# Kernel optimization log

Measured on AMD Instinct MI355X. Metric: run time of the kernel, lower is better.

Reference implementation:

```python
import jax, jax.numpy as jnp
import numpy as np

V, C, H, T, B, D = 32000, 768, 12, 1024, 2, 4
HID = C // 2
FF = 4 * C
HD = C // H


def _ln(x, s, b):
    m = jnp.mean(x, axis=-1, keepdims=True)
    v = jnp.mean((x - m) ** 2, axis=-1, keepdims=True)
    return (x - m) * jax.lax.rsqrt(v + 1e-5) * s + b


def setup_inputs() -> dict:
    key = jax.random.key(0)
    ks = jax.random.split(key, 12)
    nrm = lambda k, shp: 0.02 * jax.random.normal(k, shp, dtype=jnp.float32)
    return {
        "idx": jax.random.randint(ks[0], (B, T), 0, V),
        "tok_emb": nrm(ks[1], (V, C)),
        "pos_emb": nrm(ks[2], (T, C)),
        "r_w1": nrm(ks[3], (C, HID)), "r_b1": jnp.zeros((HID,), jnp.float32),
        "r_w2": nrm(ks[4], (HID, D)), "r_b2": jnp.zeros((D,), jnp.float32),
        "ln1_s": jnp.ones((C,), jnp.float32), "ln1_b": jnp.zeros((C,), jnp.float32),
        "qkv_w": nrm(ks[5], (C, 3 * C)),
        "proj_w": nrm(ks[6], (C, C)), "proj_b": jnp.zeros((C,), jnp.float32),
        "ln2_s": jnp.ones((C,), jnp.float32), "ln2_b": jnp.zeros((C,), jnp.float32),
        "f_w1": nrm(ks[7], (C, FF)), "f_b1": jnp.zeros((FF,), jnp.float32),
        "f_w2": nrm(ks[8], (FF, C)), "f_b2": jnp.zeros((C,), jnp.float32),
        "lnf_s": jnp.ones((C,), jnp.float32), "lnf_b": jnp.zeros((C,), jnp.float32),
        "head_w": nrm(ks[9], (V, C)),  # torch Linear weight [out, in]
    }


def reference(idx, tok_emb, pos_emb, r_w1, r_b1, r_w2, r_b2,
              ln1_s, ln1_b, qkv_w, proj_w, proj_b, ln2_s, ln2_b,
              f_w1, f_b1, f_w2, f_b2, lnf_s, lnf_b, head_w):
    # embeddings
    x = tok_emb[idx] + pos_emb[None, :, :]  # [B,T,C]

    # depth router (eval mode: hard one-hot argmax, k=1)
    rh = jax.nn.relu(x @ r_w1 + r_b1)
    r_logits = rh @ r_w2 + r_b2  # [B,T,D]
    w = jax.nn.one_hot(jnp.argmax(r_logits, axis=-1), D, dtype=x.dtype)  # [B,T,D]

    causal = jnp.tril(jnp.ones((T, T), dtype=bool))
    scale = 1.0 / np.sqrt(HD).astype(np.float32)

    def block(z):
        # pre-norm attention
        y = _ln(z, ln1_s, ln1_b)
        qkv = y @ qkv_w  # [B,T,3C]
        q, k, v = jnp.split(qkv, 3, axis=-1)
        q = q.reshape(B, T, H, HD)
        k = k.reshape(B, T, H, HD)
        v = v.reshape(B, T, H, HD)
        att = jnp.einsum('bqhd,bkhd->bhqk', q, k) * scale
        att = jnp.where(causal, att, -jnp.inf)
        att = jax.nn.softmax(att, axis=-1)
        o = jnp.einsum('bhqk,bkhd->bqhd', att, v).reshape(B, T, C)
        z = z + (o @ proj_w + proj_b)
        # pre-norm FFN (dropout inactive in eval)
        y2 = _ln(z, ln2_s, ln2_b)
        ff = jax.nn.gelu(y2 @ f_w1 + f_b1, approximate=False) @ f_w2 + f_b2
        return z + ff

    # depth-d output = block applied (d+1) times; accumulate with router weight
    out = jnp.zeros_like(x)
    h = x
    for d in range(D):
        h = block(h)
        out = out + w[:, :, d:d + 1] * h

    xf = _ln(out, lnf_s, lnf_b)
    logits = xf @ head_w.T  # [B,T,V]
    return logits
```

## Files before the change

kernel.cpp:

```cpp
#include <hip/hip_runtime.h>
#include <hip/hip_bf16.h>

typedef unsigned short u16;
typedef __bf16 bf16x8 __attribute__((ext_vector_type(8)));
typedef float f32x4 __attribute__((ext_vector_type(4)));

#define DEVINL __device__ __forceinline__

DEVINL u16 f2b(float f){
  unsigned u = __float_as_uint(f);
  u += 0x7FFFu + ((u >> 16) & 1u);
  return (u16)(u >> 16);
}
DEVINL float b2f(u16 b){ return __uint_as_float(((unsigned)b) << 16); }

DEVINL void gload16(const void* g, void* l){
  __builtin_amdgcn_global_load_lds(
      (const __attribute__((address_space(1))) unsigned*)g,
      (__attribute__((address_space(3))) unsigned*)l, 16, 0, 0);
}

__global__ __launch_bounds__(256) void k_embed(const int* __restrict__ idx,
    const float* __restrict__ tok, const float* __restrict__ pos, float* __restrict__ h){
  int r = blockIdx.x, t = threadIdx.x;
  int token = idx[r];
  const float* tr = tok + (long)token * 768;
  const float* pr = pos + (long)(r & 1023) * 768;
  float* hr = h + (long)r * 768;
  hr[t]       = tr[t]       + pr[t];
  hr[t + 256] = tr[t + 256] + pr[t + 256];
  hr[t + 512] = tr[t + 512] + pr[t + 512];
}

__global__ __launch_bounds__(256) void k_ln(const float* __restrict__ X,
    const float* __restrict__ s, const float* __restrict__ b, u16* __restrict__ Y){
  int r = blockIdx.x, t = threadIdx.x;
  const float* x = X + (long)r * 768;
  float v0 = x[t], v1 = x[t + 256], v2 = x[t + 512];
  float sum = v0 + v1 + v2;
  __shared__ float tmp[4];
  #pragma unroll
  for (int o = 32; o; o >>= 1) sum += __shfl_xor(sum, o);
  int wave = t >> 6;
  if ((t & 63) == 0) tmp[wave] = sum;
  __syncthreads();
  sum = tmp[0] + tmp[1] + tmp[2] + tmp[3];
  float m = sum * (1.f / 768.f);
  float d0 = v0 - m, d1 = v1 - m, d2 = v2 - m;
  float sq = d0 * d0 + d1 * d1 + d2 * d2;
  #pragma unroll
  for (int o = 32; o; o >>= 1) sq += __shfl_xor(sq, o);
  __syncthreads();
  if ((t & 63) == 0) tmp[wave] = sq;
  __syncthreads();
  sq = tmp[0] + tmp[1] + tmp[2] + tmp[3];
  float rs = rsqrtf(sq * (1.f / 768.f) + 1e-5f);
  u16* y = Y + (long)r * 768;
  y[t]       = f2b(d0 * rs * s[t]       + b[t]);
  y[t + 256] = f2b(d1 * rs * s[t + 256] + b[t + 256]);
  y[t + 512] = f2b(d2 * rs * s[t + 512] + b[t + 512]);
}

__global__ __launch_bounds__(256) void k_wt(const float* __restrict__ W, u16* __restrict__ Wt,
                                            int K, int N){
  __shared__ float tile[32][33];
  int kb = blockIdx.x * 32, nb = blockIdx.y * 32;
  int tx = threadIdx.x & 31, ty = threadIdx.x >> 5;
  #pragma unroll
  for (int i = 0; i < 32; i += 8) tile[ty + i][tx] = W[(long)(kb + ty + i) * N + nb + tx];
  __syncthreads();
  #pragma unroll
  for (int i = 0; i < 32; i += 8) Wt[(long)(nb + ty + i) * K + kb + tx] = f2b(tile[tx][ty + i]);
}

__global__ __launch_bounds__(256) void k_conv(const float* __restrict__ W, u16* __restrict__ O, long n4){
  long i = (long)blockIdx.x * 256 + threadIdx.x;
  if (i >= n4) return;
  float4 v = ((const float4*)W)[i];
  unsigned lo = (unsigned)f2b(v.x) | ((unsigned)f2b(v.y) << 16);
  unsigned hi = (unsigned)f2b(v.z) | ((unsigned)f2b(v.w) << 16);
  ((uint2*)O)[i] = make_uint2(lo, hi);
}

__global__ __launch_bounds__(256) void k_r1(const float* __restrict__ A, const float* __restrict__ B,
    const float* __restrict__ bias, float* __restrict__ C){
  __shared__ float As[64][17];
  __shared__ float Bs[16][65];
  int r0 = blockIdx.x * 64, c0 = blockIdx.y * 64;
  int t = threadIdx.x;
  int tx = t & 15, ty = t >> 4;
  float acc[4][4] = {};
  for (int k0 = 0; k0 < 768; k0 += 16){
    #pragma unroll
    for (int i = 0; i < 4; i++){ int e = i * 256 + t; As[e >> 4][e & 15] = A[(long)(r0 + (e >> 4)) * 768 + k0 + (e & 15)]; }
    #pragma unroll
    for (int i = 0; i < 4; i++){ int e = i * 256 + t; Bs[e >> 6][e & 63] = B[(long)(k0 + (e >> 6)) * 384 + c0 + (e & 63)]; }
    __syncthreads();
    #pragma unroll
    for (int kk = 0; kk < 16; kk++){
      float a[4], bb[4];
      #pragma unroll
      for (int i = 0; i < 4; i++) a[i] = As[ty * 4 + i][kk];
      #pragma unroll
      for (int j = 0; j < 4; j++) bb[j] = Bs[kk][tx * 4 + j];
      #pragma unroll
      for (int i = 0; i < 4; i++)
        #pragma unroll
        for (int j = 0; j < 4; j++) acc[i][j] += a[i] * bb[j];
    }
    __syncthreads();
  }
  #pragma unroll
  for (int i = 0; i < 4; i++)
    #pragma unroll
    for (int j = 0; j < 4; j++){
      int rr = r0 + ty * 4 + i, cc = c0 + tx * 4 + j;
      float v = acc[i][j] + bias[cc];
      C[(long)rr * 384 + cc] = v > 0.f ? v : 0.f;
    }
}

__global__ __launch_bounds__(64) void k_r2(const float* __restrict__ rh, const float* __restrict__ w2,
    const float* __restrict__ b2, int* __restrict__ sel){
  int tkn = blockIdx.x, l = threadIdx.x;
  float s0 = 0, s1 = 0, s2 = 0, s3 = 0;
  const float* r = rh + (long)tkn * 384;
  for (int k = l; k < 384; k += 64){
    float rv = r[k];
    float4 w = ((const float4*)w2)[k];
    s0 += rv * w.x; s1 += rv * w.y; s2 += rv * w.z; s3 += rv * w.w;
  }
  #pragma unroll
  for (int o = 32; o; o >>= 1){
    s0 += __shfl_xor(s0, o); s1 += __shfl_xor(s1, o);
    s2 += __shfl_xor(s2, o); s3 += __shfl_xor(s3, o);
  }
  if (l == 0){
    float v[4] = { s0 + b2[0], s1 + b2[1], s2 + b2[2], s3 + b2[3] };
    int am = 0; float bv = v[0];
    #pragma unroll
    for (int j = 1; j < 4; j++) if (v[j] > bv){ bv = v[j]; am = j; }
    sel[tkn] = am;
  }
}

__global__ __launch_bounds__(256) void k_attn(
    const u16* __restrict__ qkv, const u16* __restrict__ Vt, u16* __restrict__ o){
  __shared__ __align__(16) u16 Klds[64][64];
  __shared__ __align__(16) u16 Vlds[64][64];
  __shared__ __align__(16) u16 Plds[4][16][72];
  int qt = blockIdx.x, bh = blockIdx.y;
  int b = bh / 12, hh = bh % 12;
  int t = threadIdx.x, w = t >> 6, lane = t & 63;
  int lr = lane & 15, koct = lane >> 4;
  int q0 = qt * 64 + w * 16;
  const u16* Qrow = qkv + ((long)(b * 1024 + q0 + lr)) * 2304 + hh * 64;
  bf16x8 qf[2];
  qf[0] = __builtin_bit_cast(bf16x8, *(const uint4*)&Qrow[koct * 8]);
  qf[1] = __builtin_bit_cast(bf16x8, *(const uint4*)&Qrow[32 + koct * 8]);
  f32x4 oacc[4] = {};
  float m_run[4], l_run[4];
  #pragma unroll
  for (int r = 0; r < 4; r++){ m_run[r] = -1e30f; l_run[r] = 0.f; }
  int srow8 = lane >> 3, scolb = (lane & 7) * 16;
  const char* Kbase = (const char*)(qkv + (long)b * 1024 * 2304 + 768 + hh * 64);
  const char* Vbase = (const char*)(Vt + (long)bh * 64 * 1024);
  for (int kvt = 0; kvt <= qt; ++kvt){
    #pragma unroll
    for (int i = 0; i < 2; i++){
      int row = w * 16 + i * 8 + srow8;
      int sb = scolb ^ ((row & 7) << 4);
      gload16(Kbase + (long)(kvt * 64 + row) * 4608 + sb, &Klds[w * 16 + i * 8][0]);
    }
    #pragma unroll
    for (int i = 0; i < 2; i++){
      int row = w * 16 + i * 8 + srow8;
      int sb = scolb ^ ((row & 7) << 4);
      gload16(Vbase + (long)row * 2048 + kvt * 128 + sb, &Vlds[w * 16 + i * 8][0]);
    }
    __syncthreads();
    f32x4 sacc[4] = {};
    #pragma unroll
    for (int j = 0; j < 4; j++){
      #pragma unroll
      for (int f = 0; f < 2; f++){
        int row = 16 * j + lr;
        bf16x8 kf = __builtin_bit_cast(bf16x8, *(const uint4*)(
            (const char*)&Klds[0][0] + row * 128 + ((64 * f + koct * 16) ^ ((row & 7) << 4))));
        sacc[j] = __builtin_amdgcn_mfma_f32_16x16x32_bf16(qf[f], kf, sacc[j], 0, 0, 0);
      }
    }
    bool diag = (kvt == qt);
    float p[4][4];
    #pragma unroll
    for (int r = 0; r < 4; r++){
      int qg = q0 + 4 * koct + r;
      float vj[4];
      #pragma unroll
      for (int j = 0; j < 4; j++){
        int kvg = kvt * 64 + 16 * j + lr;
        float v = sacc[j][r] * 0.125f;
        vj[j] = (!diag || kvg <= qg) ? v : -1e30f;
      }
      float mx = fmaxf(fmaxf(vj[0], vj[1]), fmaxf(vj[2], vj[3]));
      #pragma unroll
      for (int s = 1; s < 16; s <<= 1) mx = fmaxf(mx, __shfl_xor(mx, s));
      float mn = fmaxf(m_run[r], mx);
      float sc = __expf(m_run[r] - mn);
      float rs = 0.f;
      #pragma unroll
      for (int j = 0; j < 4; j++){ p[j][r] = __expf(vj[j] - mn); rs += p[j][r]; }
      #pragma unroll
      for (int s = 1; s < 16; s <<= 1) rs += __shfl_xor(rs, s);
      l_run[r] = l_run[r] * sc + rs;
      m_run[r] = mn;
      #pragma unroll
      for (int j = 0; j < 4; j++) oacc[j][r] *= sc;
    }
    #pragma unroll
    for (int r = 0; r < 4; r++)
      #pragma unroll
      for (int j = 0; j < 4; j++)
        Plds[w][4 * koct + r][16 * j + lr] = f2b(p[j][r]);
    bf16x8 pf[2];
    pf[0] = __builtin_bit_cast(bf16x8, *(const uint4*)&Plds[w][lr][koct * 8]);
    pf[1] = __builtin_bit_cast(bf16x8, *(const uint4*)&Plds[w][lr][32 + koct * 8]);
    #pragma unroll
    for (int j = 0; j < 4; j++){
      #pragma unroll
      for (int f = 0; f < 2; f++){
        int row = 16 * j + lr;
        bf16x8 vf = __builtin_bit_cast(bf16x8, *(const uint4*)(
            (const char*)&Vlds[0][0] + row * 128 + ((64 * f + koct * 16) ^ ((row & 7) << 4))));
        oacc[j] = __builtin_amdgcn_mfma_f32_16x16x32_bf16(pf[f], vf, oacc[j], 0, 0, 0);
      }
    }
    __syncthreads();
  }
  float inv[4];
  #pragma unroll
  for (int r = 0; r < 4; r++) inv[r] = 1.f / l_run[r];
  #pragma unroll
  for (int j = 0; j < 4; j++){
    #pragma unroll
    for (int r = 0; r < 4; r++){
      int tq = b * 1024 + q0 + 4 * koct + r;
      o[(long)tq * 768 + hh * 64 + 16 * j + lr] = f2b(oacc[j][r] * inv[r]);
    }
  }
}

__global__ __launch_bounds__(256) void k_redln(const float* __restrict__ P, int nparts,
    const float* __restrict__ bias, const float* __restrict__ resid, float* __restrict__ outh,
    const float* __restrict__ ls, const float* __restrict__ lb, u16* __restrict__ Y,
    const int* __restrict__ sel, float* __restrict__ outb, int d){
  int r = blockIdx.x, t = threadIdx.x;
  float v0, v1, v2;
  {
    float a0 = bias[t]       + resid[(long)r * 768 + t];
    float a1 = bias[t + 256] + resid[(long)r * 768 + t + 256];
    float a2 = bias[t + 512] + resid[(long)r * 768 + t + 512];
    for (int p = 0; p < nparts; p++){
      const float* pr = P + ((long)p * 2048 + r) * 768;
      a0 += pr[t]; a1 += pr[t + 256]; a2 += pr[t + 512];
    }
    v0 = a0; v1 = a1; v2 = a2;
  }
  float* hr = outh + (long)r * 768;
  hr[t] = v0; hr[t + 256] = v1; hr[t + 512] = v2;
  if (sel && sel[r] == d){
    float* orow = outb + (long)r * 768;
    orow[t] = v0; orow[t + 256] = v1; orow[t + 512] = v2;
  }
  float sum = v0 + v1 + v2;
  __shared__ float tmp[4];
  #pragma unroll
  for (int o = 32; o; o >>= 1) sum += __shfl_xor(sum, o);
  int wave = t >> 6;
  if ((t & 63) == 0) tmp[wave] = sum;
  __syncthreads();
  sum = tmp[0] + tmp[1] + tmp[2] + tmp[3];
  float m = sum * (1.f / 768.f);
  float d0 = v0 - m, d1 = v1 - m, d2 = v2 - m;
  float sq = d0 * d0 + d1 * d1 + d2 * d2;
  #pragma unroll
  for (int o = 32; o; o >>= 1) sq += __shfl_xor(sq, o);
  __syncthreads();
  if ((t & 63) == 0) tmp[wave] = sq;
  __syncthreads();
  sq = tmp[0] + tmp[1] + tmp[2] + tmp[3];
  float rs = rsqrtf(sq * (1.f / 768.f) + 1e-5f);
  u16* y = Y + (long)r * 768;
  y[t]       = f2b(d0 * rs * ls[t]       + lb[t]);
  y[t + 256] = f2b(d1 * rs * ls[t + 256] + lb[t + 256]);
  y[t + 512] = f2b(d2 * rs * ls[t + 512] + lb[t + 512]);
}

__global__ __launch_bounds__(64) void k_gemm1(
    const u16* __restrict__ A, int lda, long s1A, long s2A,
    const u16* __restrict__ B, int ldb, long s1B, long s2B,
    void* Cv, int ldc, long s1C, long s2C,
    const float* __restrict__ bias,
    const float* __restrict__ resid, int ldr,
    int K, int zdiv, int ksegK, int flags, u16* __restrict__ vtbuf){
  __shared__ __align__(16) u16 As[2][64][32];
  __shared__ __align__(16) u16 Bs[2][64][32];
  int lane = threadIdx.x;
  int bx = blockIdx.x, by = blockIdx.y, bz = blockIdx.z;
  if (flags & 16){
    int nx = gridDim.x, nwg = nx * gridDim.y;
    int lin = by * nx + bx;
    int q = nwg >> 3;
    int nl = (lin & 7) * q + (lin >> 3);
    bx = nl % nx; by = nl / nx;
  }
  int row0 = bx * 64, col0 = by * 64;
  int zq = bz / zdiv, zr = bz % zdiv;
  A += zq * s2A + (long)zr * s1A;
  B += zq * s2B + (long)zr * s1B;
  long coff = zq * s2C + (long)zr * s1C;
  int kstart = 0, Klim = K;
  if (ksegK > 0){ kstart = bz * ksegK; Klim = kstart + ksegK; }
  f32x4 acc[4][4] = {};
  int lr = lane & 15, lk = (lane >> 4) * 8;
  int srow = lane >> 2, scol = (lane & 3) * 16;
  int nt = (Klim - kstart) >> 5;
  auto STAGE = [&](int buf, int k0){
    #pragma unroll
    for (int i = 0; i < 4; i++)
      gload16((const char*)&A[(long)(row0 + i * 16 + srow) * lda + k0] + scol, &As[buf][i * 16][0]);
    #pragma unroll
    for (int i = 0; i < 4; i++)
      gload16((const char*)&B[(long)(col0 + i * 16 + srow) * ldb + k0] + scol, &Bs[buf][i * 16][0]);
  };
  STAGE(0, kstart);
  int cur = 0;
  for (int t = 0; t < nt; t++){
    if (t + 1 < nt){
      STAGE(cur ^ 1, kstart + ((t + 1) << 5));
      asm volatile("s_waitcnt vmcnt(8)" ::: "memory");
    } else {
      asm volatile("s_waitcnt vmcnt(0)" ::: "memory");
    }
    __builtin_amdgcn_sched_barrier(0);
    bf16x8 af[4], bb[4];
    #pragma unroll
    for (int i = 0; i < 4; i++)
      af[i] = __builtin_bit_cast(bf16x8, *(const uint4*)&As[cur][i * 16 + lr][lk]);
    #pragma unroll
    for (int j = 0; j < 4; j++)
      bb[j] = __builtin_bit_cast(bf16x8, *(const uint4*)&Bs[cur][j * 16 + lr][lk]);
    #pragma unroll
    for (int i = 0; i < 4; i++)
      #pragma unroll
      for (int j = 0; j < 4; j++)
        acc[i][j] = __builtin_amdgcn_mfma_f32_16x16x32_bf16(af[i], bb[j], acc[i][j], 0, 0, 0);
    __builtin_amdgcn_sched_barrier(0);
    cur ^= 1;
  }
  bool vmode = (vtbuf != nullptr) && (col0 >= 1536);
  if (vmode){
    #pragma unroll
    for (int i = 0; i < 4; i++){
      int rbase = row0 + i * 16 + ((lane >> 4) << 2);
      int b = rbase >> 10, tt = rbase & 1023;
      #pragma unroll
      for (int j = 0; j < 4; j++){
        int cc = col0 + j * 16 + lr;
        int hh = (cc - 1536) >> 6, dd = (cc - 1536) & 63;
        unsigned lo = (unsigned)f2b(acc[i][j][0]) | ((unsigned)f2b(acc[i][j][1]) << 16);
        unsigned hi = (unsigned)f2b(acc[i][j][2]) | ((unsigned)f2b(acc[i][j][3]) << 16);
        *(uint2*)&vtbuf[((long)(b * 12 + hh) * 64 + dd) * 1024 + tt] = make_uint2(lo, hi);
      }
    }
    return;
  }
  #pragma unroll
  for (int i = 0; i < 4; i++){
    int rbase = row0 + i * 16 + ((lane >> 4) << 2);
    #pragma unroll
    for (int j = 0; j < 4; j++){
      int cc = col0 + j * 16 + lr;
      #pragma unroll
      for (int q = 0; q < 4; q++){
        int rr = rbase + q;
        float v = acc[i][j][q];
        if (bias) v += bias[cc];
        if (flags & 2) v = 0.5f * v * (1.f + erff(v * 0.70710678118654752f));
        if (resid) v += resid[(long)rr * ldr + cc];
        if (flags & 1) ((u16*)Cv)[coff + (long)rr * ldc + cc] = f2b(v);
        else           ((float*)Cv)[coff + (long)rr * ldc + cc] = v;
      }
    }
  }
}

__global__ __launch_bounds__(512, 2) void k_head(
    const u16* __restrict__ A, const u16* __restrict__ B, float* __restrict__ C){
  __shared__ __align__(16) u16 As[2][256][64];
  __shared__ __align__(16) u16 Bs[2][256][64];
  const int lda = 768, ldb = 768, ldc = 32000;
  int t = threadIdx.x, w = t >> 6, lane = t & 63;
  int wm = w >> 2, wn = w & 3;
  int bx = blockIdx.x, by = blockIdx.y;
  {
    int nx = gridDim.x, nwg = nx * gridDim.y;
    int lin = by * nx + bx;
    int q = nwg >> 3;
    int nl = (lin & 7) * q + (lin >> 3);
    bx = nl % nx; by = nl / nx;
  }
  long row0 = (long)bx * 256, col0 = (long)by * 256;
  int srow = lane >> 3;
  int scolb = (lane & 7) * 16;
  int lr = lane & 15, koct = lane >> 4;
  f32x4 acc[8][4] = {};
  const int nt = 12;
  auto STAGE_A = [&](int buf, int k0){
    #pragma unroll
    for (int g = 0; g < 4; g++){
      int row = g * 64 + w * 8 + srow;
      gload16((const char*)&A[(row0 + row) * lda + k0] + (scolb ^ ((row & 7) << 4)),
              &As[buf][g * 64 + w * 8][0]);
    }
  };
  auto STAGE_B = [&](int buf, int k0){
    #pragma unroll
    for (int g = 0; g < 4; g++){
      int row = g * 64 + w * 8 + srow;
      gload16((const char*)&B[(col0 + row) * ldb + k0] + (scolb ^ ((row & 7) << 4)),
              &Bs[buf][g * 64 + w * 8][0]);
    }
  };
  STAGE_A(0, 0);
  STAGE_B(0, 0);
  int cur = 0;
  for (int kt = 0; kt < nt; kt++){
    bool more = kt + 1 < nt;
    if (more){
      STAGE_A(cur ^ 1, (kt + 1) * 64);
      asm volatile("s_waitcnt vmcnt(4)" ::: "memory");
    } else {
      asm volatile("s_waitcnt vmcnt(0)" ::: "memory");
    }
    __builtin_amdgcn_sched_barrier(0);
    __syncthreads();
    #pragma unroll
    for (int s = 0; s < 2; s++){
      bf16x8 af[8], bfr[4];
      #pragma unroll
      for (int i = 0; i < 8; i++){
        int row = wm * 128 + i * 16 + lr;
        af[i] = __builtin_bit_cast(bf16x8, *(const uint4*)(
            (const char*)&As[cur][0][0] + row * 128 + ((s * 64 + koct * 16) ^ ((row & 7) << 4))));
      }
      #pragma unroll
      for (int j = 0; j < 4; j++){
        int row = wn * 64 + j * 16 + lr;
        bfr[j] = __builtin_bit_cast(bf16x8, *(const uint4*)(
            (const char*)&Bs[cur][0][0] + row * 128 + ((s * 64 + koct * 16) ^ ((row & 7) << 4))));
      }
      if (s == 0 && more) STAGE_B(cur ^ 1, (kt + 1) * 64);
      __builtin_amdgcn_s_setprio(1);
      #pragma unroll
      for (int i = 0; i < 8; i++)
        #pragma unroll
        for (int j = 0; j < 4; j++)
          acc[i][j] = __builtin_amdgcn_mfma_f32_16x16x32_bf16(af[i], bfr[j], acc[i][j], 0, 0, 0);
      __builtin_amdgcn_s_setprio(0);
    }
    __syncthreads();
    cur ^= 1;
  }
  #pragma unroll
  for (int i = 0; i < 8; i++){
    long rbase = row0 + wm * 128 + i * 16 + koct * 4;
    #pragma unroll
    for (int j = 0; j < 4; j++){
      long cc = col0 + wn * 64 + j * 16 + lr;
      #pragma unroll
      for (int q = 0; q < 4; q++)
        C[(rbase + q) * ldc + cc] = acc[i][j][q];
    }
  }
}

extern "C" void kernel_launch(void* const* d_in, const int* in_sizes, int n_in,
                              void* d_out, int out_size, void* d_ws, size_t ws_size,
                              hipStream_t stream){
  const int*   idx    = (const int*)d_in[0];
  const float* tok    = (const float*)d_in[1];
  const float* pos    = (const float*)d_in[2];
  const float* r_w1   = (const float*)d_in[3];
  const float* r_b1   = (const float*)d_in[4];
  const float* r_w2   = (const float*)d_in[5];
  const float* r_b2   = (const float*)d_in[6];
  const float* ln1_s  = (const float*)d_in[7];
  const float* ln1_b  = (const float*)d_in[8];
  const float* qkv_w  = (const float*)d_in[9];
  const float* proj_w = (const float*)d_in[10];
  const float* proj_b = (const float*)d_in[11];
  const float* ln2_s  = (const float*)d_in[12];
  const float* ln2_b  = (const float*)d_in[13];
  const float* f_w1   = (const float*)d_in[14];
  const float* f_b1   = (const float*)d_in[15];
  const float* f_w2   = (const float*)d_in[16];
  const float* f_b2   = (const float*)d_in[17];
  const float* lnf_s  = (const float*)d_in[18];
  const float* lnf_b  = (const float*)d_in[19];
  const float* head_w = (const float*)d_in[20];
  float* logits = (float*)d_out;

  char* w = (char*)d_ws;
  size_t off = 0;
  auto alloc = [&](size_t bytes)->char*{ char* p = w + off; off += (bytes + 255) & ~(size_t)255; return p; };
  u16*   wqT  = (u16*)  alloc(2304ull * 768 * 2);
  u16*   wpT  = (u16*)  alloc(768ull * 768 * 2);
  u16*   wf1T = (u16*)  alloc(3072ull * 768 * 2);
  u16*   wf2T = (u16*)  alloc(768ull * 3072 * 2);
  u16*   whd  = (u16*)  alloc(32000ull * 768 * 2);
  float* h    = (float*)alloc(2048ull * 768 * 4);
  float* outb = (float*)alloc(2048ull * 768 * 4);
  u16*   y    = (u16*)  alloc(2048ull * 768 * 2);
  u16*   qkv  = (u16*)  alloc(2048ull * 2304 * 2);
  u16*   o    = (u16*)  alloc(2048ull * 768 * 2);
  u16*   ffh  = (u16*)  alloc(2048ull * 3072 * 2);
  u16*   Vt   = (u16*)  alloc(24ull * 64 * 1024 * 2);
  float* rh   = (float*)alloc(2048ull * 384 * 4);
  int*   sel  = (int*)  alloc(2048 * 4);
  float* Sf   = (float*)alloc(4ull * 2048 * 768 * 4);
  (void)in_sizes; (void)n_in; (void)out_size; (void)ws_size;

  dim3 b256(256), b64(64);
  k_wt<<<dim3(24, 72), b256, 0, stream>>>(qkv_w,  wqT,  768, 2304);
  k_wt<<<dim3(24, 24), b256, 0, stream>>>(proj_w, wpT,  768, 768);
  k_wt<<<dim3(24, 96), b256, 0, stream>>>(f_w1,   wf1T, 768, 3072);
  k_wt<<<dim3(96, 24), b256, 0, stream>>>(f_w2,   wf2T, 3072, 768);
  k_conv<<<24000, b256, 0, stream>>>(head_w, whd, 6144000);
  k_embed<<<2048, b256, 0, stream>>>(idx, tok, pos, h);
  k_r1<<<dim3(32, 6), b256, 0, stream>>>(h, r_w1, r_b1, rh);
  k_r2<<<2048, b64, 0, stream>>>(rh, r_w2, r_b2, sel);
  k_ln<<<2048, b256, 0, stream>>>(h, ln1_s, ln1_b, y);

  for (int d = 0; d < 4; ++d){
    k_gemm1<<<dim3(32, 36), b64, 0, stream>>>(
        y, 768, 0, 0, wqT, 768, 0, 0, qkv, 2304, 0, 0,
        nullptr, nullptr, 0, 768, 12, 0, 1 | 16, Vt);
    k_attn<<<dim3(16, 24), b256, 0, stream>>>(qkv, Vt, o);
    k_gemm1<<<dim3(32, 12, 2), b64, 0, stream>>>(
        o, 768, 0, 0, wpT, 768, 0, 0, Sf, 768, 2048ll * 768, 0,
        nullptr, nullptr, 0, 768, 12, 384, 16, nullptr);
    k_redln<<<2048, b256, 0, stream>>>(Sf, 2, proj_b, h, h, ln2_s, ln2_b, y,
                                       nullptr, nullptr, 0);
    k_gemm1<<<dim3(32, 48), b64, 0, stream>>>(
        y, 768, 0, 0, wf1T, 768, 0, 0, ffh, 3072, 0, 0,
        f_b1, nullptr, 0, 768, 12, 0, 1 | 2 | 16, nullptr);
    k_gemm1<<<dim3(32, 12, 4), b64, 0, stream>>>(
        ffh, 3072, 0, 0, wf2T, 3072, 0, 0, Sf, 768, 2048ll * 768, 0,
        nullptr, nullptr, 0, 3072, 12, 768, 16, nullptr);
    k_redln<<<2048, b256, 0, stream>>>(Sf, 4, f_b2, h, h, ln1_s, ln1_b, y,
                                       sel, outb, d);
  }
  k_ln<<<2048, b256, 0, stream>>>(outb, lnf_s, lnf_b, y);
  k_head<<<dim3(8, 125), dim3(512), 0, stream>>>(y, whd, logits);
}
```

Baseline: 895.8 us.

## Replace head kernel and QKV/FF1 GEMMs with shared 128x128 four-wave GEMM

Adds a generic 128x128-tile, 256-thread MFMA GEMM with a bias/GELU/bf16 epilogue and a V-transpose mode. It replaces the single-wave k_gemm1 launches for QKV and FF1, and also the 256x256 double-buffered k_head kernel. The goal is larger tiles and more LDS reuse for the per-layer GEMMs. The cost is that the LM head loses double buffering and its bigger tile, and the new kernel has no load/compute overlap since each k step loads synchronously.

```diff
diff --git a/kernel.cpp b/kernel.cpp
--- a/kernel.cpp
+++ b/kernel.cpp
@@ -395,92 +395,95 @@
   }
 }
 
-__global__ __launch_bounds__(512, 2) void k_head(
-    const u16* __restrict__ A, const u16* __restrict__ B, float* __restrict__ C){
-  __shared__ __align__(16) u16 As[2][256][64];
-  __shared__ __align__(16) u16 Bs[2][256][64];
-  const int lda = 768, ldb = 768, ldc = 32000;
+__global__ __launch_bounds__(256) void k_gemm4(
+    const u16* __restrict__ A, int lda,
+    const u16* __restrict__ B, int ldb,
+    void* Cv, int ldc,
+    const float* __restrict__ bias, int K, int flags, u16* __restrict__ vtbuf){
+  __shared__ __align__(16) u16 As[128][64];
+  __shared__ __align__(16) u16 Bs[128][64];
   int t = threadIdx.x, w = t >> 6, lane = t & 63;
-  int wm = w >> 2, wn = w & 3;
+  int wm = w >> 1, wn = w & 1;
   int bx = blockIdx.x, by = blockIdx.y;
-  {
+  if (flags & 16){
     int nx = gridDim.x, nwg = nx * gridDim.y;
     int lin = by * nx + bx;
     int q = nwg >> 3;
     int nl = (lin & 7) * q + (lin >> 3);
     bx = nl % nx; by = nl / nx;
   }
-  long row0 = (long)bx * 256, col0 = (long)by * 256;
-  int srow = lane >> 3;
-  int scolb = (lane & 7) * 16;
+  long row0 = (long)bx * 128, col0 = (long)by * 128;
+  int srow = lane >> 3, scolb = (lane & 7) * 16;
   int lr = lane & 15, koct = lane >> 4;
-  f32x4 acc[8][4] = {};
-  const int nt = 12;
-  auto STAGE_A = [&](int buf, int k0){
+  f32x4 acc[4][4] = {};
+  for (int k0 = 0; k0 < K; k0 += 64){
     #pragma unroll
     for (int g = 0; g < 4; g++){
-      int row = g * 64 + w * 8 + srow;
+      int row = g * 32 + w * 8 + srow;
       gload16((const char*)&A[(row0 + row) * lda + k0] + (scolb ^ ((row & 7) << 4)),
-              &As[buf][g * 64 + w * 8][0]);
-    }
-  };
-  auto STAGE_B = [&](int buf, int k0){
+              &As[g * 32 + w * 8][0]);
+    }
     #pragma unroll
     for (int g = 0; g < 4; g++){
-      int row = g * 64 + w * 8 + srow;
+      int row = g * 32 + w * 8 + srow;
       gload16((const char*)&B[(col0 + row) * ldb + k0] + (scolb ^ ((row & 7) << 4)),
-              &Bs[buf][g * 64 + w * 8][0]);
-    }
-  };
-  STAGE_A(0, 0);
-  STAGE_B(0, 0);
-  int cur = 0;
-  for (int kt = 0; kt < nt; kt++){
-    bool more = kt + 1 < nt;
-    if (more){
-      STAGE_A(cur ^ 1, (kt + 1) * 64);
-      asm volatile("s_waitcnt vmcnt(4)" ::: "memory");
-    } else {
-      asm volatile("s_waitcnt vmcnt(0)" ::: "memory");
-    }
-    __builtin_amdgcn_sched_barrier(0);
+              &Bs[g * 32 + w * 8][0]);
+    }
     __syncthreads();
     #pragma unroll
     for (int s = 0; s < 2; s++){
-      bf16x8 af[8], bfr[4];
-      #pragma unroll
-      for (int i = 0; i < 8; i++){
-        int row = wm * 128 + i * 16 + lr;
+      bf16x8 af[4], bfr[4];
+      #pragma unroll
+      for (int i = 0; i < 4; i++){
+        int row = wm * 64 + i * 16 + lr;
         af[i] = __builtin_bit_cast(bf16x8, *(const uint4*)(
-            (const char*)&As[cur][0][0] + row * 128 + ((s * 64 + koct * 16) ^ ((row & 7) << 4))));
+            (const char*)&As[0][0] + row * 128 + ((s * 64 + koct * 16) ^ ((row & 7) << 4))));
       }
       #pragma unroll
       for (int j = 0; j < 4; j++){
         int row = wn * 64 + j * 16 + lr;
         bfr[j] = __builtin_bit_cast(bf16x8, *(const uint4*)(
-            (const char*)&Bs[cur][0][0] + row * 128 + ((s * 64 + koct * 16) ^ ((row & 7) << 4))));
-      }
-      if (s == 0 && more) STAGE_B(cur ^ 1, (kt + 1) * 64);
-      __builtin_amdgcn_s_setprio(1);
-      #pragma unroll
-      for (int i = 0; i < 8; i++)
+            (const char*)&Bs[0][0] + row * 128 + ((s * 64 + koct * 16) ^ ((row & 7) << 4))));
+      }
+      #pragma unroll
+      for (int i = 0; i < 4; i++)
         #pragma unroll
         for (int j = 0; j < 4; j++)
           acc[i][j] = __builtin_amdgcn_mfma_f32_16x16x32_bf16(af[i], bfr[j], acc[i][j], 0, 0, 0);
-      __builtin_amdgcn_s_setprio(0);
     }
     __syncthreads();
-    cur ^= 1;
-  }
-  #pragma unroll
-  for (int i = 0; i < 8; i++){
-    long rbase = row0 + wm * 128 + i * 16 + koct * 4;
+  }
+  bool vmode = (vtbuf != nullptr) && (col0 >= 1536);
+  if (vmode){
+    #pragma unroll
+    for (int i = 0; i < 4; i++){
+      long rbase = row0 + wm * 64 + i * 16 + koct * 4;
+      int b = (int)(rbase >> 10), tt = (int)(rbase & 1023);
+      #pragma unroll
+      for (int j = 0; j < 4; j++){
+        long cc = col0 + wn * 64 + j * 16 + lr;
+        int hh = (int)((cc - 1536) >> 6), dd = (int)((cc - 1536) & 63);
+        unsigned lo = (unsigned)f2b(acc[i][j][0]) | ((unsigned)f2b(acc[i][j][1]) << 16);
+        unsigned hi = (unsigned)f2b(acc[i][j][2]) | ((unsigned)f2b(acc[i][j][3]) << 16);
+        *(uint2*)&vtbuf[((long)(b * 12 + hh) * 64 + dd) * 1024 + tt] = make_uint2(lo, hi);
+      }
+    }
+    return;
+  }
+  #pragma unroll
+  for (int i = 0; i < 4; i++){
+    long rbase = row0 + wm * 64 + i * 16 + koct * 4;
     #pragma unroll
     for (int j = 0; j < 4; j++){
       long cc = col0 + wn * 64 + j * 16 + lr;
       #pragma unroll
-      for (int q = 0; q < 4; q++)
-        C[(rbase + q) * ldc + cc] = acc[i][j][q];
+      for (int q = 0; q < 4; q++){
+        float v = acc[i][j][q];
+        if (bias) v += bias[cc];
+        if (flags & 2) v = 0.5f * v * (1.f + erff(v * 0.70710678118654752f));
+        if (flags & 1) ((u16*)Cv)[(rbase + q) * ldc + cc] = f2b(v);
+        else           ((float*)Cv)[(rbase + q) * ldc + cc] = v;
+      }
     }
   }
 }
@@ -543,18 +546,16 @@
   k_ln<<<2048, b256, 0, stream>>>(h, ln1_s, ln1_b, y);
 
   for (int d = 0; d < 4; ++d){
-    k_gemm1<<<dim3(32, 36), b64, 0, stream>>>(
-        y, 768, 0, 0, wqT, 768, 0, 0, qkv, 2304, 0, 0,
-        nullptr, nullptr, 0, 768, 12, 0, 1 | 16, Vt);
+    k_gemm4<<<dim3(16, 18), b256, 0, stream>>>(
+        y, 768, wqT, 768, qkv, 2304, nullptr, 768, 1 | 16, Vt);
     k_attn<<<dim3(16, 24), b256, 0, stream>>>(qkv, Vt, o);
     k_gemm1<<<dim3(32, 12, 2), b64, 0, stream>>>(
         o, 768, 0, 0, wpT, 768, 0, 0, Sf, 768, 2048ll * 768, 0,
         nullptr, nullptr, 0, 768, 12, 384, 16, nullptr);
     k_redln<<<2048, b256, 0, stream>>>(Sf, 2, proj_b, h, h, ln2_s, ln2_b, y,
                                        nullptr, nullptr, 0);
-    k_gemm1<<<dim3(32, 48), b64, 0, stream>>>(
-        y, 768, 0, 0, wf1T, 768, 0, 0, ffh, 3072, 0, 0,
-        f_b1, nullptr, 0, 768, 12, 0, 1 | 2 | 16, nullptr);
+    k_gemm4<<<dim3(16, 24), b256, 0, stream>>>(
+        y, 768, wf1T, 768, ffh, 3072, f_b1, 768, 1 | 2 | 16, nullptr);
     k_gemm1<<<dim3(32, 12, 4), b64, 0, stream>>>(
         ffh, 3072, 0, 0, wf2T, 3072, 0, 0, Sf, 768, 2048ll * 768, 0,
         nullptr, nullptr, 0, 3072, 12, 768, 16, nullptr);
@@ -562,5 +563,6 @@
                                        sel, outb, d);
   }
   k_ln<<<2048, b256, 0, stream>>>(outb, lnf_s, lnf_b, y);
-  k_head<<<dim3(8, 125), dim3(512), 0, stream>>>(y, whd, logits);
-}
+  k_gemm4<<<dim3(16, 250), b256, 0, stream>>>(
+      y, 768, whd, 768, logits, 32000, nullptr, 768, 16, nullptr);
+}
```

Result: slower. 998.0 us (+11.4%).
